# Optimization experiments

Measured on AMD Instinct MI355X. Metric: run time of the kernel, lower is better.

Reference implementation:

```python
import jax, jax.numpy as jnp
import numpy as np

N, L, D, H = 4, 2048, 1024, 16
HD = D // H  # head_dim = 64


def setup_inputs() -> dict:
    key = jax.random.key(0)
    ks = jax.random.split(key, 6)
    x = jax.random.normal(ks[0], (N, L, D), dtype=jnp.float32)
    mask = jax.random.randint(ks[1], (N, L), 0, 2).astype(bool)
    W_qkv = jax.random.normal(ks[2], (3 * D, D), dtype=jnp.float32) * (1.0 / np.sqrt(D))
    b_qkv = jax.random.normal(ks[3], (3 * D,), dtype=jnp.float32) * 0.02
    W_out = jax.random.normal(ks[4], (D, D), dtype=jnp.float32) * (1.0 / np.sqrt(D))
    b_out = jax.random.normal(ks[5], (D,), dtype=jnp.float32) * 0.02
    return {"x": x, "mask": mask, "W_qkv": W_qkv, "b_qkv": b_qkv,
            "W_out": W_out, "b_out": b_out}


def reference(x, mask, W_qkv, b_qkv, W_out, b_out):
    # qkv projection: torch Linear is y = x @ W.T + b
    qkv = jnp.einsum('nld,ed->nle', x, W_qkv) + b_qkv          # [N, L, 3D]
    q, k, v = jnp.split(qkv, 3, axis=-1)                        # each [N, L, D]
    # [N, L, D] -> [N, H, L, HD]
    to_heads = lambda t: t.reshape(N, L, H, HD).transpose(0, 2, 1, 3)
    q, k, v = to_heads(q), to_heads(k), to_heads(v)
    scale = 1.0 / np.sqrt(HD)
    scores = jnp.einsum('nhqd,nhkd->nhqk', q, k) * scale        # [N, H, L, L]
    # faithful to source: masked_fill where mask is True -> -1e9
    scores = jnp.where(mask[:, None, None, :], -1e9, scores)
    attn = jax.nn.softmax(scores, axis=-1)                      # dropout = identity (eval)
    out = jnp.einsum('nhqk,nhkd->nhqd', attn, v)                # [N, H, L, HD]
    out = out.transpose(0, 2, 1, 3).reshape(N, L, D)
    return jnp.einsum('nld,ed->nle', out, W_out) + b_out
```

## Files before the change

kernel.cpp:

```cpp
#include <hip/hip_runtime.h>
#include <hip/hip_bf16.h>
#include <cmath>

#define NB   4
#define LL   2048
#define DD   1024
#define HH   16
#define HD   64

typedef __bf16 bf16;
typedef __bf16 bf16x4 __attribute__((ext_vector_type(4)));
typedef __bf16 bf16x8 __attribute__((ext_vector_type(8)));
typedef float  f32x4  __attribute__((ext_vector_type(4)));
typedef float  f32x8  __attribute__((ext_vector_type(8)));

__device__ __forceinline__ void gload16(void* lds_base, const void* gsrc) {
    __builtin_amdgcn_global_load_lds(
        (const __attribute__((address_space(1))) unsigned int*)gsrc,
        (__attribute__((address_space(3))) unsigned int*)lds_base, 16, 0, 0);
}

__global__ __launch_bounds__(1024) void mask_prep(const unsigned char* __restrict__ mraw,
                                                  float* __restrict__ maskB) {
    __shared__ int anyOdd;
    if (threadIdx.x == 0) anyOdd = 0;
    __syncthreads();
    const int base = blockIdx.x * 1024;
    const int i = base + threadIdx.x;
    if ((i & 3) != 0 && mraw[i] != 0) atomicOr(&anyOdd, 1);
    __syncthreads();
    const bool isBytes = (anyOdd != 0);
    int v = isBytes ? (int)mraw[i] : ((const int*)mraw)[i];
    maskB[i] = v ? -1.4426950408889634e9f : -12.0f;
}

__global__ __launch_bounds__(256) void cast_f32_bf16(const float* __restrict__ src,
                                                     bf16* __restrict__ dst, int n8) {
    const int i = blockIdx.x * 256 + threadIdx.x;
    if (i >= n8) return;
    const float4* s = (const float4*)src + (size_t)i * 2;
    float4 a = s[0], b = s[1];
    bf16x8 o;
    o[0] = (bf16)a.x; o[1] = (bf16)a.y; o[2] = (bf16)a.z; o[3] = (bf16)a.w;
    o[4] = (bf16)b.x; o[5] = (bf16)b.y; o[6] = (bf16)b.z; o[7] = (bf16)b.w;
    *((bf16x8*)dst + i) = o;
}

template <int EPI>
__global__ __launch_bounds__(256) void gemm_mfma(const bf16* __restrict__ A,
                                                 const bf16* __restrict__ B,
                                                 const float* __restrict__ bias,
                                                 void* __restrict__ C0v,
                                                 void* __restrict__ C1v,
                                                 void* __restrict__ C2v,
                                                 int M, int N, int K) {
    __shared__ __attribute__((aligned(16))) char As[128 * 64];
    __shared__ __attribute__((aligned(16))) char Bs[128 * 64];

    const int tid = threadIdx.x;
    const int wave = tid >> 6;
    const int lane = tid & 63;
    const int kl = lane & 15;
    const int h = lane >> 4;
    const int wm = wave >> 1;
    const int wn = wave & 1;
    const int m0 = blockIdx.y * 128;
    const int n0 = blockIdx.x * 128;

    f32x4 acc[4][4];
#pragma unroll
    for (int i = 0; i < 4; ++i)
#pragma unroll
        for (int j = 0; j < 4; ++j) acc[i][j] = (f32x4){0.f, 0.f, 0.f, 0.f};

    const int sr = wave * 16 + (lane >> 2);
    const int sc = (lane & 3) * 16;
    const char* A0 = (const char*)A + ((size_t)(m0 + sr) * K) * 2 + sc;
    const char* A1 = (const char*)A + ((size_t)(m0 + 64 + sr) * K) * 2 + sc;
    const char* B0 = (const char*)B + ((size_t)(n0 + sr) * K) * 2 + sc;
    const char* B1 = (const char*)B + ((size_t)(n0 + 64 + sr) * K) * 2 + sc;
    char* AsD = As + wave * 1024;
    char* BsD = Bs + wave * 1024;

    for (int kt = 0; kt < K; kt += 32) {
        __syncthreads();
        gload16(AsD,        A0 + kt * 2);
        gload16(AsD + 4096, A1 + kt * 2);
        gload16(BsD,        B0 + kt * 2);
        gload16(BsD + 4096, B1 + kt * 2);
        asm volatile("s_waitcnt vmcnt(0)" ::: "memory");
        __syncthreads();

        bf16x8 a[4], b[4];
#pragma unroll
        for (int mt = 0; mt < 4; ++mt)
            a[mt] = *(const bf16x8*)(As + (wm * 64 + mt * 16 + kl) * 64 + h * 16);
#pragma unroll
        for (int nt = 0; nt < 4; ++nt)
            b[nt] = *(const bf16x8*)(Bs + (wn * 64 + nt * 16 + kl) * 64 + h * 16);
#pragma unroll
        for (int mt = 0; mt < 4; ++mt)
#pragma unroll
            for (int nt = 0; nt < 4; ++nt)
                acc[mt][nt] = __builtin_amdgcn_mfma_f32_16x16x32_bf16(a[mt], b[nt], acc[mt][nt], 0, 0, 0);
    }

    if (EPI == 1) {
        float* C0 = (float*)C0v;
#pragma unroll
        for (int mt = 0; mt < 4; ++mt) {
            const int mb = m0 + wm * 64 + mt * 16 + 4 * h;
#pragma unroll
            for (int nt = 0; nt < 4; ++nt) {
                const int n = n0 + wn * 64 + nt * 16 + kl;
                const float bv = bias[n];
#pragma unroll
                for (int r = 0; r < 4; ++r)
                    C0[(size_t)(mb + r) * N + n] = acc[mt][nt][r] + bv;
            }
        }
    } else {
        const int which = n0 >> 10;
        if (which < 2) {
            bf16* dst = (which == 0) ? (bf16*)C0v : (bf16*)C1v;
#pragma unroll
            for (int mt = 0; mt < 4; ++mt) {
                const int mb = m0 + wm * 64 + mt * 16 + 4 * h;
#pragma unroll
                for (int nt = 0; nt < 4; ++nt) {
                    const int gn = n0 + wn * 64 + nt * 16 + kl;
                    const float bv = bias[gn];
                    const int nn = gn & 1023;
                    const int hh = nn >> 6;
                    const int d = nn & 63;
#pragma unroll
                    for (int r = 0; r < 4; ++r) {
                        const int m = mb + r;
                        const int n_ = m >> 11;
                        const int l_ = m & 2047;
                        dst[((size_t)(n_ * HH + hh) * LL + l_) * HD + d] = (bf16)(acc[mt][nt][r] + bv);
                    }
                }
            }
        } else {
            bf16* dst = (bf16*)C2v;
#pragma unroll
            for (int mt = 0; mt < 4; ++mt) {
                const int mb = m0 + wm * 64 + mt * 16 + 4 * h;
                const int n_ = mb >> 11;
                const int l0 = mb & 2047;
#pragma unroll
                for (int nt = 0; nt < 4; ++nt) {
                    const int gn = n0 + wn * 64 + nt * 16 + kl;
                    const float bv = bias[gn];
                    const int nn = gn & 1023;
                    const int hh = nn >> 6;
                    const int d = nn & 63;
                    bf16x4 o4;
#pragma unroll
                    for (int r = 0; r < 4; ++r) o4[r] = (bf16)(acc[mt][nt][r] + bv);
                    *(bf16x4*)(dst + ((size_t)(n_ * HH + hh) * HD + d) * LL + l0) = o4;
                }
            }
        }
    }
}

#define SWZ3(row) ((((row) & 3) | ((((row) >> 3) & 1) << 2)) << 4)

__global__ __launch_bounds__(512) void attn_mfma(const bf16* __restrict__ Qg,
                                                 const bf16* __restrict__ Kg,
                                                 const bf16* __restrict__ VTg,
                                                 const float* __restrict__ maskB,
                                                 bf16* __restrict__ Oout) {
    __shared__ __attribute__((aligned(16))) char KtB0[8192];
    __shared__ __attribute__((aligned(16))) char KtB1[8192];
    __shared__ __attribute__((aligned(16))) char VtB0[8192];
    __shared__ __attribute__((aligned(16))) char VtB1[8192];

    const int tid = threadIdx.x;
    const int wave = tid >> 6;
    const int lane = tid & 63;
    const int kl = lane & 15;
    const int h = lane >> 4;

    const int f = blockIdx.x;
    const int qb = (f >> 3) & 7;
    const int bh = (f & 7) | ((f >> 6) << 3);
    const int n_ = bh >> 4;
    const int hh = bh & 15;
    const int q0 = qb * 256 + wave * 32;

    bf16x8 qf[2][2];
#pragma unroll
    for (int qt = 0; qt < 2; ++qt)
#pragma unroll
        for (int st = 0; st < 2; ++st)
            qf[qt][st] = *(const bf16x8*)(Qg + (((size_t)bh * LL + q0 + qt * 16 + kl) * HD + st * 32 + h * 8));

    f32x4 Oa[2][4];
    f32x4 Osum[2];
#pragma unroll
    for (int qt = 0; qt < 2; ++qt) {
        Osum[qt] = (f32x4){0.f, 0.f, 0.f, 0.f};
#pragma unroll
        for (int t = 0; t < 4; ++t) Oa[qt][t] = (f32x4){0.f, 0.f, 0.f, 0.f};
    }

    bf16x8 ones;
#pragma unroll
    for (int j = 0; j < 8; ++j) ones[j] = (bf16)1.0f;

    int koff[2][2][2];
#pragma unroll
    for (int c = 0; c < 2; ++c) {
        const int r1 = c * 32 + ((kl >> 2) << 3) + (kl & 3);
        const int r2 = r1 + 4;
#pragma unroll
        for (int st = 0; st < 2; ++st) {
            koff[c][0][st] = r1 * 128 + ((st * 64 + h * 16) ^ SWZ3(r1));
            koff[c][1][st] = r2 * 128 + ((st * 64 + h * 16) ^ SWZ3(r2));
        }
    }
    int voff[2][4];
#pragma unroll
    for (int c = 0; c < 2; ++c)
#pragma unroll
        for (int tt = 0; tt < 4; ++tt) {
            const int row = tt * 16 + kl;
            voff[c][tt] = row * 128 + ((c * 64 + h * 16) ^ SWZ3(row));
        }

    const int rA = wave * 8 + (lane >> 3);
    const int swA = ((lane & 7) << 4) ^ SWZ3(rA);
    const char* Kb = (const char*)Kg + (size_t)bh * LL * 128;
    const char* Vb = (const char*)VTg + (size_t)bh * HD * (LL * 2);
    const char* kSA = Kb + (size_t)rA * 128 + swA;
    const char* vSA = Vb + (size_t)rA * 4096 + swA;

    const float* mptr = maskB + n_ * LL + h * 8;
    const float scale = 0.18033688011f;

#define STAGE_TO(KT, VT, k0s)                                   \
    do {                                                        \
        gload16((KT) + wave * 1024, kSA + (size_t)(k0s) * 128); \
        gload16((VT) + wave * 1024, vSA + (k0s) * 2);           \
    } while (0)

#define LOADMK(MK, k0s)                                                      \
    do {                                                                     \
        _Pragma("unroll") for (int c = 0; c < 2; ++c)                        \
            _Pragma("unroll") for (int f2 = 0; f2 < 2; ++f2)                 \
                MK[c][f2] = *(const f32x4*)(mptr + (k0s) + c * 32 + f2 * 4); \
    } while (0)

#define COMPUTE(KT, VT, MK)                                                            \
    do {                                                                               \
        bf16x8 kf[2][2][2], vf[2][4];                                                  \
        _Pragma("unroll") for (int c = 0; c < 2; ++c)                                  \
            _Pragma("unroll") for (int fr = 0; fr < 2; ++fr)                           \
                _Pragma("unroll") for (int st = 0; st < 2; ++st)                       \
                    kf[c][fr][st] = *(const bf16x8*)((KT) + koff[c][fr][st]);          \
        __builtin_amdgcn_sched_barrier(0);             \
        _Pragma("unroll") for (int c = 0; c < 2; ++c)                                  \
            _Pragma("unroll") for (int tt = 0; tt < 4; ++tt)                           \
                vf[c][tt] = *(const bf16x8*)((VT) + voff[c][tt]);                      \
        asm volatile("s_waitcnt lgkmcnt(8)" ::: "memory");                \
        __builtin_amdgcn_sched_barrier(0);                                             \
        bf16x8 pa[2][2];                                                               \
        _Pragma("unroll") for (int qt = 0; qt < 2; ++qt) {                             \
            f32x4 sv[2][2];                                                            \
            _Pragma("unroll") for (int c = 0; c < 2; ++c)                              \
                _Pragma("unroll") for (int fr = 0; fr < 2; ++fr) {                     \
                    f32x4 z = {0.f, 0.f, 0.f, 0.f};                                    \
                    f32x4 a = __builtin_amdgcn_mfma_f32_16x16x32_bf16(kf[c][fr][0],    \
                                                         qf[qt][0], z, 0, 0, 0);       \
                    sv[c][fr] = __builtin_amdgcn_mfma_f32_16x16x32_bf16(kf[c][fr][1],  \
                                                         qf[qt][1], a, 0, 0, 0);       \
                }                                                                      \
            _Pragma("unroll") for (int c = 0; c < 2; ++c) {                            \
                f32x8 pf;                                                              \
                _Pragma("unroll") for (int f2 = 0; f2 < 2; ++f2) {                     \
                    f32x4 s = sv[c][f2] * scale + MK[c][f2];                           \
                    _Pragma("unroll") for (int r = 0; r < 4; ++r)                      \
                        pf[f2 * 4 + r] = __builtin_amdgcn_exp2f(s[r]);                 \
                }                                                                      \
                pa[qt][c] = __builtin_convertvector(pf, bf16x8);                       \
            }                                                                          \
        }                                                                              \
        asm volatile("s_waitcnt lgkmcnt(0)" ::: "memory");                \
        __builtin_amdgcn_sched_barrier(0);                                             \
        _Pragma("unroll") for (int qt = 0; qt < 2; ++qt) {                             \
            Osum[qt] = __builtin_amdgcn_mfma_f32_16x16x32_bf16(pa[qt][0], ones,        \
                                                               Osum[qt], 0, 0, 0);     \
            Osum[qt] = __builtin_amdgcn_mfma_f32_16x16x32_bf16(pa[qt][1], ones,        \
                                                               Osum[qt], 0, 0, 0);     \
            _Pragma("unroll") for (int c = 0; c < 2; ++c)                              \
                _Pragma("unroll") for (int tt = 0; tt < 4; ++tt)                       \
                    Oa[qt][tt] = __builtin_amdgcn_mfma_f32_16x16x32_bf16(pa[qt][c],    \
                                                 vf[c][tt], Oa[qt][tt], 0, 0, 0);      \
        }                                                                              \
    } while (0)

    f32x4 mkA[2][2], mkB[2][2];

    LOADMK(mkA, 0);
    STAGE_TO(KtB0, VtB0, 0);
    asm volatile("s_waitcnt vmcnt(0)" ::: "memory");
    __builtin_amdgcn_s_barrier();

    for (int t = 0; t < 32; t += 2) {
        STAGE_TO(KtB1, VtB1, (t + 1) * 64);
        __builtin_amdgcn_sched_barrier(0);
        LOADMK(mkB, (t + 1) * 64);
        COMPUTE(KtB0, VtB0, mkA);
        asm volatile("s_waitcnt vmcnt(4)" ::: "memory");
        __builtin_amdgcn_s_barrier();

        if (t + 2 < 32) {
            STAGE_TO(KtB0, VtB0, (t + 2) * 64);
            __builtin_amdgcn_sched_barrier(0);
            LOADMK(mkA, (t + 2) * 64);
            COMPUTE(KtB1, VtB1, mkB);
            asm volatile("s_waitcnt vmcnt(4)" ::: "memory");
            __builtin_amdgcn_s_barrier();
        } else {
            COMPUTE(KtB1, VtB1, mkB);
        }
    }

#pragma unroll
    for (int qt = 0; qt < 2; ++qt) {
#pragma unroll
        for (int r = 0; r < 4; ++r) {
            const float inv = 1.0f / Osum[qt][r];
            const int qrow = q0 + qt * 16 + h * 4 + r;
#pragma unroll
            for (int tt = 0; tt < 4; ++tt)
                Oout[((size_t)n_ * LL + qrow) * DD + hh * HD + tt * 16 + kl] =
                    (bf16)(Oa[qt][tt][r] * inv);
        }
    }
#undef STAGE_TO
#undef LOADMK
#undef COMPUTE
}

extern "C" void kernel_launch(void* const* d_in, const int* in_sizes, int n_in,
                              void* d_out, int out_size, void* d_ws, size_t ws_size,
                              hipStream_t stream) {
    const float* x     = (const float*)d_in[0];
    const void*  mask  = d_in[1];
    const float* W_qkv = (const float*)d_in[2];
    const float* b_qkv = (const float*)d_in[3];
    const float* W_out = (const float*)d_in[4];
    const float* b_out = (const float*)d_in[5];
    float* out = (float*)d_out;

    char* ws = (char*)d_ws;
    float* maskB = (float*)ws;
    bf16*  xb    = (bf16*)(ws + (1ull  << 20));
    bf16*  wqb   = (bf16*)(ws + (18ull << 20));
    bf16*  wob   = (bf16*)(ws + (25ull << 20));
    bf16*  qb    = (bf16*)(ws + (28ull << 20));
    bf16*  kb    = (bf16*)(ws + (45ull << 20));
    bf16*  vtb   = (bf16*)(ws + (62ull << 20));
    bf16*  attnb = (bf16*)(ws + (79ull << 20));

    mask_prep<<<8, 1024, 0, stream>>>((const unsigned char*)mask, maskB);

    cast_f32_bf16<<<(NB * LL * DD / 8) / 256, 256, 0, stream>>>(x, xb, NB * LL * DD / 8);
    cast_f32_bf16<<<(3 * DD * DD / 8) / 256, 256, 0, stream>>>(W_qkv, wqb, 3 * DD * DD / 8);
    cast_f32_bf16<<<(DD * DD / 8) / 256, 256, 0, stream>>>(W_out, wob, DD * DD / 8);

    gemm_mfma<0><<<dim3(3 * DD / 128, NB * LL / 128), 256, 0, stream>>>(
        xb, wqb, b_qkv, qb, kb, vtb, NB * LL, 3 * DD, DD);

    attn_mfma<<<512, 512, 0, stream>>>(qb, kb, vtb, maskB, attnb);

    gemm_mfma<1><<<dim3(DD / 128, NB * LL / 128), 256, 0, stream>>>(
        attnb, wob, b_out, out, nullptr, nullptr, NB * LL, DD, DD);
}
```

Measured before the change: 208.1 us.

## Double-buffer LDS tiles in the bf16 MFMA GEMM to overlap loads with compute

Splits each GEMM shared-memory tile into two ping-pong buffers. The next K-slice is issued with async global-to-LDS loads while MFMAs run on the current slice. Each step needs only one barrier instead of two, and the loop is fully unrolled in pairs. The trip count is hardcoded to 32, which matches K=1024, and LDS use doubles, which may lower occupancy.

```diff
diff --git a/kernel.cpp b/kernel.cpp
--- a/kernel.cpp
+++ b/kernel.cpp
@@ -54,8 +54,10 @@
                                                  void* __restrict__ C1v,
                                                  void* __restrict__ C2v,
                                                  int M, int N, int K) {
-    __shared__ __attribute__((aligned(16))) char As[128 * 64];
-    __shared__ __attribute__((aligned(16))) char Bs[128 * 64];
+    __shared__ __attribute__((aligned(16))) char As0[8192];
+    __shared__ __attribute__((aligned(16))) char As1[8192];
+    __shared__ __attribute__((aligned(16))) char Bs0[8192];
+    __shared__ __attribute__((aligned(16))) char Bs1[8192];
 
     const int tid = threadIdx.x;
     const int wave = tid >> 6;
@@ -79,31 +81,51 @@
     const char* A1 = (const char*)A + ((size_t)(m0 + 64 + sr) * K) * 2 + sc;
     const char* B0 = (const char*)B + ((size_t)(n0 + sr) * K) * 2 + sc;
     const char* B1 = (const char*)B + ((size_t)(n0 + 64 + sr) * K) * 2 + sc;
-    char* AsD = As + wave * 1024;
-    char* BsD = Bs + wave * 1024;
-
-    for (int kt = 0; kt < K; kt += 32) {
-        __syncthreads();
-        gload16(AsD,        A0 + kt * 2);
-        gload16(AsD + 4096, A1 + kt * 2);
-        gload16(BsD,        B0 + kt * 2);
-        gload16(BsD + 4096, B1 + kt * 2);
+    const int wofs = wave * 1024;
+
+#define GSTAGE(AS, BS, kt)                          \
+    do {                                            \
+        gload16((AS) + wofs,        A0 + (kt) * 2); \
+        gload16((AS) + wofs + 4096, A1 + (kt) * 2); \
+        gload16((BS) + wofs,        B0 + (kt) * 2); \
+        gload16((BS) + wofs + 4096, B1 + (kt) * 2); \
+    } while (0)
+
+#define GCOMPUTE(AS, BS)                                                           \
+    do {                                                                           \
+        bf16x8 a[4], b[4];                                                         \
+        _Pragma("unroll") for (int mt = 0; mt < 4; ++mt)                           \
+            a[mt] = *(const bf16x8*)((AS) + (wm * 64 + mt * 16 + kl) * 64 + h * 16); \
+        _Pragma("unroll") for (int nt = 0; nt < 4; ++nt)                           \
+            b[nt] = *(const bf16x8*)((BS) + (wn * 64 + nt * 16 + kl) * 64 + h * 16); \
+        _Pragma("unroll") for (int mt = 0; mt < 4; ++mt)                           \
+            _Pragma("unroll") for (int nt = 0; nt < 4; ++nt)                       \
+                acc[mt][nt] = __builtin_amdgcn_mfma_f32_16x16x32_bf16(             \
+                    a[mt], b[nt], acc[mt][nt], 0, 0, 0);                           \
+    } while (0)
+
+    GSTAGE(As0, Bs0, 0);
+    asm volatile("s_waitcnt vmcnt(0)" ::: "memory");
+    __builtin_amdgcn_s_barrier();
+
+    for (int t = 0; t < 32; t += 2) {
+        GSTAGE(As1, Bs1, (t + 1) * 32);
+        __builtin_amdgcn_sched_barrier(0);
+        GCOMPUTE(As0, Bs0);
         asm volatile("s_waitcnt vmcnt(0)" ::: "memory");
-        __syncthreads();
-
-        bf16x8 a[4], b[4];
-#pragma unroll
-        for (int mt = 0; mt < 4; ++mt)
-            a[mt] = *(const bf16x8*)(As + (wm * 64 + mt * 16 + kl) * 64 + h * 16);
-#pragma unroll
-        for (int nt = 0; nt < 4; ++nt)
-            b[nt] = *(const bf16x8*)(Bs + (wn * 64 + nt * 16 + kl) * 64 + h * 16);
-#pragma unroll
-        for (int mt = 0; mt < 4; ++mt)
-#pragma unroll
-            for (int nt = 0; nt < 4; ++nt)
-                acc[mt][nt] = __builtin_amdgcn_mfma_f32_16x16x32_bf16(a[mt], b[nt], acc[mt][nt], 0, 0, 0);
-    }
+        __builtin_amdgcn_s_barrier();
+        if (t + 2 < 32) {
+            GSTAGE(As0, Bs0, (t + 2) * 32);
+            __builtin_amdgcn_sched_barrier(0);
+            GCOMPUTE(As1, Bs1);
+            asm volatile("s_waitcnt vmcnt(0)" ::: "memory");
+            __builtin_amdgcn_s_barrier();
+        } else {
+            GCOMPUTE(As1, Bs1);
+        }
+    }
+#undef GSTAGE
+#undef GCOMPUTE
 
     if (EPI == 1) {
         float* C0 = (float*)C0v;
```

Result: faster. 202.9 us (-2.5%).
